# Kernel tuning notes

Hardware: AMD Instinct MI355X
Metric: run time of the kernel (lower is better)

Reference implementation:

```python
import jax, jax.numpy as jnp
import numpy as np

M = 65536
INPUT_DIM = 16
OUTPUT_DIM = 64
N = 32          # coordinates transformed by the spline
K = 16          # number of spline bins
MIN_BW = 0.001  # DEFAULT_MIN_BIN_WIDTH
MIN_BH = 0.001  # DEFAULT_MIN_BIN_HEIGHT


def setup_inputs() -> dict:
    key = jax.random.key(0)
    k1, k2, k3, k4 = jax.random.split(key, 4)
    c = jax.random.uniform(k1, (M, INPUT_DIM), jnp.float32)
    z = jax.random.uniform(k2, (M, OUTPUT_DIM), jnp.float32)  # data in [0,1] spline domain
    s_in = OUTPUT_DIM - N + INPUT_DIM  # 48
    s_out = N * (2 * K + 1)            # 1056
    W = jax.random.normal(k3, (s_in, s_out), jnp.float32) * 0.05
    b = jax.random.normal(k4, (s_out,), jnp.float32) * 0.05
    return {"c": c, "z": z, "W": W, "b": b}


def _quadratic_spline(inputs, unnormalized_widths, unnormalized_heights):
    # inputs: [m, n] in [0,1]; unnormalized_widths: [m, n, K]; unnormalized_heights: [m, n, K+1]
    num_bins = unnormalized_widths.shape[-1]

    widths = jax.nn.softmax(unnormalized_widths, axis=-1)
    widths = MIN_BW + (1.0 - MIN_BW * num_bins) * widths

    h = jax.nn.softplus(unnormalized_heights) + 0.001  # [m, n, K+1]
    # (heights have K+1 = num_bins+1 knots, so the 'num_bins-1' padding branch is skipped)
    area = jnp.sum((h[..., :-1] + h[..., 1:]) * 0.5 * widths, axis=-1, keepdims=True)
    heights = h / area
    heights = MIN_BH + (1.0 - MIN_BH) * heights

    cdf = jnp.cumsum((heights[..., :-1] + heights[..., 1:]) * 0.5 * widths, axis=-1)
    cdf = cdf.at[..., -1].set(1.0)
    bin_left_cdf = jnp.pad(cdf, ((0, 0), (0, 0), (1, 0)))  # [m, n, K+1]

    locs = jnp.cumsum(widths, axis=-1).at[..., -1].set(1.0)
    bin_locations = jnp.pad(locs, ((0, 0), (0, 0), (1, 0)))  # [m, n, K+1]

    # nflows torchutils.searchsorted: bump last knot by eps, count knots <= input
    locs_eps = bin_locations.at[..., -1].add(1e-6)
    bin_idx = jnp.sum(inputs[..., None] >= locs_eps, axis=-1) - 1  # [m, n] int

    def gather(arr, idx):
        return jnp.take_along_axis(arr, idx[..., None], axis=-1)[..., 0]

    input_bin_locations = gather(bin_locations, bin_idx)
    input_bin_widths = gather(widths, bin_idx)
    input_left_cdf = gather(bin_left_cdf, bin_idx)
    input_left_heights = gather(heights, bin_idx)
    input_right_heights = gather(heights, bin_idx + 1)

    a = 0.5 * (input_right_heights - input_left_heights) * input_bin_widths
    bq = input_left_heights * input_bin_widths
    cq = input_left_cdf

    alpha = (inputs - input_bin_locations) / input_bin_widths
    outputs = jnp.clip(a * alpha ** 2 + bq * alpha + cq, 0.0, 1.0)
    logabsdet = jnp.log(alpha * (input_right_heights - input_left_heights) + input_left_heights)
    return outputs, logabsdet


def reference(c, z, W, b):
    # forward (reverse=False) branch of QuadraticsSpline.forward
    z1, z2 = z[:, :N], z[:, N:]
    z2c = jnp.concatenate([z2, c], axis=1)
    y = z2c @ W + b                                  # conditioner s (linear)
    sv = y.reshape(y.shape[0], N, 2 * K + 1)
    unnormalized_heights = sv[..., : K + 1]          # first split chunk (size K+1)
    unnormalized_widths = sv[..., K + 1:]            # second chunk (size K)
    x1, log_det = _quadratic_spline(z1, unnormalized_widths, unnormalized_heights)
    x = jnp.concatenate([z2, x1], axis=1)            # note: original concatenates (x2, x1)
    return x, log_det.sum(axis=1)
```

## Files before the change

### kernel.cpp

```cpp
#include <hip/hip_runtime.h>
#include <hip/hip_bf16.h>
#include <math.h>

#define M_ROWS 65536
#define NSPLINE 32
#define BM 64
#define WROWS 16
#define GROUP 4
#define NITER (NSPLINE / GROUP)
#define NTILE 9
#define WB_ELEMS (NITER * NTILE * 2 * 64 * 8)

typedef __attribute__((ext_vector_type(8))) _Float16 half8;
typedef __attribute__((ext_vector_type(4))) float floatx4;

__device__ __forceinline__ float softplus_fast(float t) {
    float u = t * t;
    if (u > 1.21f) return log1pf(__expf(t));
    float p = fmaf(u, -2.6352e-5f, 3.4722222e-4f);
    p = fmaf(u, p, -5.2083333e-3f);
    p = fmaf(u, p, 0.125f);
    p = fmaf(u, p, 0.69314718f);
    return fmaf(t, 0.5f, p);
}

__global__ void pack_W(const float* __restrict__ W, const float* __restrict__ b,
                       _Float16* __restrict__ WH) {
    int idx = blockIdx.x * 256 + threadIdx.x;
    int j    = idx & 7;
    int lane = (idx >> 3) & 63;
    int half = (idx >> 9) & 1;
    int tile = idx >> 10;
    int tau  = tile % NTILE;
    int g    = tile / NTILE;
    int m  = lane & 15;
    int k  = half * 32 + ((lane >> 4) << 3) + j;
    int spline = g * 4 + (m >> 2);
    int param  = tau * 4 + (m & 3);
    float v = 0.0f;
    if (param < 33 && k <= 48) {
        int col = spline * 33 + param;
        v = (k < 48) ? W[k * 1056 + col] : b[col];
    }
    WH[idx] = (_Float16)v;
}

#define PV(p) (acc[(p) >> 2][(p) & 3])

__global__ void __launch_bounds__(256, 5) fused_kernel(
    const float* __restrict__ z, const float* __restrict__ c,
    const _Float16* __restrict__ WH, float* __restrict__ out)
{
    const int tid  = threadIdx.x;
    const int w    = tid >> 6;
    const int lane = tid & 63;
    const int q    = lane >> 4;
    const int cc   = lane & 15;
    const int row_base = blockIdx.x * BM + w * WROWS;

    #pragma unroll
    for (int it = 0; it < 2; ++it) {
        int idx = it * 64 + lane;
        int rr  = row_base + (idx >> 3);
        int v4  = idx & 7;
        float4 val = *(const float4*)(z + (size_t)rr * 64 + 32 + v4 * 4);
        *(float4*)(out + (size_t)rr * 64 + v4 * 4) = val;
    }

    half8 a0, a1;
    {
        const float* zr = z + (size_t)(row_base + cc) * 64 + 32;
        float4 v0 = *(const float4*)(zr + q * 8);
        float4 v1 = *(const float4*)(zr + q * 8 + 4);
        a0[0]=(_Float16)v0.x; a0[1]=(_Float16)v0.y;
        a0[2]=(_Float16)v0.z; a0[3]=(_Float16)v0.w;
        a0[4]=(_Float16)v1.x; a0[5]=(_Float16)v1.y;
        a0[6]=(_Float16)v1.z; a0[7]=(_Float16)v1.w;
        if (q < 2) {
            const float* cr = c + (size_t)(row_base + cc) * 16 + q * 8;
            float4 u0 = *(const float4*)cr;
            float4 u1 = *(const float4*)(cr + 4);
            a1[0]=(_Float16)u0.x; a1[1]=(_Float16)u0.y;
            a1[2]=(_Float16)u0.z; a1[3]=(_Float16)u0.w;
            a1[4]=(_Float16)u1.x; a1[5]=(_Float16)u1.y;
            a1[6]=(_Float16)u1.z; a1[7]=(_Float16)u1.w;
        } else {
            #pragma unroll
            for (int j = 0; j < 8; ++j) a1[j] = (_Float16)0.0f;
            if (q == 2) a1[0] = (_Float16)1.0f;
        }
    }

    const float* z1p = z + (size_t)(row_base + cc) * 64 + q;

    float ld_acc = 0.0f;

    #pragma unroll 1
    for (int g = 0; g < NITER; ++g) {
        const float in = z1p[g * 4];

        floatx4 acc[NTILE];
        const half8* base = (const half8*)WH + (size_t)g * (NTILE * 2 * 64) + lane;
        #pragma unroll
        for (int t = 0; t < NTILE; ++t) {
            half8 w0 = base[(t * 2 + 0) * 64];
            half8 w1 = base[(t * 2 + 1) * 64];
            floatx4 a = {0.f, 0.f, 0.f, 0.f};
            a = __builtin_amdgcn_mfma_f32_16x16x32_f16(w0, a0, a, 0, 0, 0);
            a = __builtin_amdgcn_mfma_f32_16x16x32_f16(w1, a1, a, 0, 0, 0);
            acc[t] = a;
        }

        const int n = g * GROUP + q;

        float wd[16];
        float sew = 0.f;
        #pragma unroll
        for (int i = 0; i < 16; ++i) {
            float e = __expf(PV(17 + i));
            wd[i] = e; sew += e;
        }
        const float inv_sew = 0.984f * __builtin_amdgcn_rcpf(sew);
        #pragma unroll
        for (int i = 0; i < 16; ++i) wd[i] = 0.001f + wd[i] * inv_sew;

        float h[17];
        #pragma unroll
        for (int i = 0; i < 17; ++i)
            h[i] = softplus_fast(PV(i)) + 0.001f;

        float area = 0.f;
        #pragma unroll
        for (int i = 0; i < 16; ++i) area += (h[i] + h[i + 1]) * 0.5f * wd[i];
        const float inv_area = 0.999f * __builtin_amdgcn_rcpf(area);
        #pragma unroll
        for (int i = 0; i < 17; ++i) h[i] = 0.001f + h[i] * inv_area;

        float loc = 0.f, cdfl = 0.f;
        float sel_loc = 0.f, sel_w = wd[0], sel_cdf = 0.f;
        float sel_lh = h[0], sel_rh = h[1];
        #pragma unroll
        for (int bn = 1; bn < 16; ++bn) {
            cdfl = fmaf((h[bn - 1] + h[bn]) * 0.5f, wd[bn - 1], cdfl);
            loc += wd[bn - 1];
            if (in >= loc) {
                sel_loc = loc; sel_w = wd[bn]; sel_cdf = cdfl;
                sel_lh = h[bn]; sel_rh = h[bn + 1];
            }
        }

        const float alpha = (in - sel_loc) * __builtin_amdgcn_rcpf(sel_w);
        const float dh    = sel_rh - sel_lh;
        float o = ((0.5f * dh * sel_w) * alpha + sel_lh * sel_w) * alpha + sel_cdf;
        o = fminf(fmaxf(o, 0.0f), 1.0f);
        out[(size_t)(row_base + cc) * 64 + 32 + n] = o;
        ld_acc += __logf(fmaf(alpha, dh, sel_lh));
    }

    ld_acc += __shfl_down(ld_acc, 32, 64);
    ld_acc += __shfl_down(ld_acc, 16, 64);
    if (q == 0)
        out[(size_t)M_ROWS * 64 + row_base + cc] = ld_acc;
}

extern "C" void kernel_launch(void* const* d_in, const int* in_sizes, int n_in,
                              void* d_out, int out_size, void* d_ws, size_t ws_size,
                              hipStream_t stream) {
    const float* c = (const float*)d_in[0];
    const float* z = (const float*)d_in[1];
    const float* W = (const float*)d_in[2];
    const float* b = (const float*)d_in[3];
    float* out = (float*)d_out;
    _Float16* WH = (_Float16*)d_ws;

    pack_W<<<WB_ELEMS / 256, 256, 0, stream>>>(W, b, WH);
    fused_kernel<<<M_ROWS / BM, 256, 0, stream>>>(z, c, WH, out);
}
```

Measured before the change: 111.5 us.

## Fold log2e into weights, rescale heights by half, stagger W tile order per wave

Width logits are pre-scaled by log2(e) in the packed weights so the softmax can use the native exp2. Heights are kept at half scale (u = h/2), which removes the 0.5 multiplies in the area and CDF sums, and the log-determinant uses native log2 with a single ln2 rescale and a constant 32*ln2 offset at the end. Each wave starts the spline-group loop at a different offset so that waves in a block read different weight tiles at the same time. The launch-bounds occupancy hint is also dropped. These changes cut VALU instruction count and spread out weight-cache traffic, but they slightly change the floating-point rounding.

Measured after the change: 128.7 us. 1.15x slower.

```diff
diff --git a/kernel.cpp b/kernel.cpp
--- a/kernel.cpp
+++ b/kernel.cpp
@@ -10,6 +10,8 @@
 #define NITER (NSPLINE / GROUP)
 #define NTILE 9
 #define WB_ELEMS (NITER * NTILE * 2 * 64 * 8)
+#define LOG2E 1.4426950408889634f
+#define LN2   0.69314718055994531f
 
 typedef __attribute__((ext_vector_type(8))) _Float16 half8;
 typedef __attribute__((ext_vector_type(4))) float floatx4;
@@ -41,13 +43,14 @@
     if (param < 33 && k <= 48) {
         int col = spline * 33 + param;
         v = (k < 48) ? W[k * 1056 + col] : b[col];
+        if (param >= 17) v *= LOG2E;
     }
     WH[idx] = (_Float16)v;
 }
 
 #define PV(p) (acc[(p) >> 2][(p) & 3])
 
-__global__ void __launch_bounds__(256, 5) fused_kernel(
+__global__ void __launch_bounds__(256) fused_kernel(
     const float* __restrict__ z, const float* __restrict__ c,
     const _Float16* __restrict__ WH, float* __restrict__ out)
 {
@@ -96,7 +99,8 @@
     float ld_acc = 0.0f;
 
     #pragma unroll 1
-    for (int g = 0; g < NITER; ++g) {
+    for (int g2 = 0; g2 < NITER; ++g2) {
+        const int g = (g2 + 2 * w) & 7;
         const float in = z1p[g * 4];
 
         floatx4 acc[NTILE];
@@ -117,50 +121,53 @@
         float sew = 0.f;
         #pragma unroll
         for (int i = 0; i < 16; ++i) {
-            float e = __expf(PV(17 + i));
+            float e = __builtin_amdgcn_exp2f(PV(17 + i));
             wd[i] = e; sew += e;
         }
         const float inv_sew = 0.984f * __builtin_amdgcn_rcpf(sew);
         #pragma unroll
         for (int i = 0; i < 16; ++i) wd[i] = 0.001f + wd[i] * inv_sew;
 
-        float h[17];
+        float hp[17];
         #pragma unroll
         for (int i = 0; i < 17; ++i)
-            h[i] = softplus_fast(PV(i)) + 0.001f;
+            hp[i] = softplus_fast(PV(i)) + 0.001f;
 
-        float area = 0.f;
+        float S = 0.f;
         #pragma unroll
-        for (int i = 0; i < 16; ++i) area += (h[i] + h[i + 1]) * 0.5f * wd[i];
-        const float inv_area = 0.999f * __builtin_amdgcn_rcpf(area);
+        for (int i = 0; i < 16; ++i) S = fmaf(hp[i] + hp[i + 1], wd[i], S);
+        const float inv2 = 0.999f * __builtin_amdgcn_rcpf(S);
+        float u[17];
         #pragma unroll
-        for (int i = 0; i < 17; ++i) h[i] = 0.001f + h[i] * inv_area;
+        for (int i = 0; i < 17; ++i) u[i] = fmaf(hp[i], inv2, 0.0005f);
 
         float loc = 0.f, cdfl = 0.f;
         float sel_loc = 0.f, sel_w = wd[0], sel_cdf = 0.f;
-        float sel_lh = h[0], sel_rh = h[1];
+        float sel_lu = u[0], sel_ru = u[1];
         #pragma unroll
         for (int bn = 1; bn < 16; ++bn) {
-            cdfl = fmaf((h[bn - 1] + h[bn]) * 0.5f, wd[bn - 1], cdfl);
+            cdfl = fmaf(u[bn - 1] + u[bn], wd[bn - 1], cdfl);
             loc += wd[bn - 1];
             if (in >= loc) {
                 sel_loc = loc; sel_w = wd[bn]; sel_cdf = cdfl;
-                sel_lh = h[bn]; sel_rh = h[bn + 1];
+                sel_lu = u[bn]; sel_ru = u[bn + 1];
             }
         }
 
         const float alpha = (in - sel_loc) * __builtin_amdgcn_rcpf(sel_w);
-        const float dh    = sel_rh - sel_lh;
-        float o = ((0.5f * dh * sel_w) * alpha + sel_lh * sel_w) * alpha + sel_cdf;
+        const float du    = sel_ru - sel_lu;
+        const float lw    = sel_lu * sel_w;
+        float o = fmaf(fmaf(du * sel_w, alpha, lw + lw), alpha, sel_cdf);
         o = fminf(fmaxf(o, 0.0f), 1.0f);
         out[(size_t)(row_base + cc) * 64 + 32 + n] = o;
-        ld_acc += __logf(fmaf(alpha, dh, sel_lh));
+        ld_acc += __builtin_amdgcn_logf(fmaf(alpha, du, sel_lu));
     }
 
     ld_acc += __shfl_down(ld_acc, 32, 64);
     ld_acc += __shfl_down(ld_acc, 16, 64);
     if (q == 0)
-        out[(size_t)M_ROWS * 64 + row_base + cc] = ld_acc;
+        out[(size_t)M_ROWS * 64 + row_base + cc] =
+            fmaf(ld_acc, LN2, 32.0f * LN2);
 }
 
 extern "C" void kernel_launch(void* const* d_in, const int* in_sizes, int n_in,
```
